# Performance work log

Measured on AMD Instinct MI355X. Metric: run time of the kernel, lower is better.

## Reference

```python
import jax, jax.numpy as jnp
import numpy as np

H = 1024
L = 2

def setup_inputs() -> dict:
    key = jax.random.key(0)
    k1, k2, k3, k4, k5 = jax.random.split(key, 5)
    B, S = 32, 2048
    scale = 1.0 / np.sqrt(H)
    return {
        "query": jax.random.normal(k1, (B, 1, H * L), dtype=jnp.float32),
        "keys": jax.random.normal(k2, (B, S, H), dtype=jnp.float32),
        "Wa_w": jax.random.normal(k3, (H * L, H), dtype=jnp.float32) * scale,
        "Wa_b": jnp.zeros((H,), dtype=jnp.float32),
        "Ua_w": jax.random.normal(k4, (H, H), dtype=jnp.float32) * scale,
        "Ua_b": jnp.zeros((H,), dtype=jnp.float32),
        "Va_w": jax.random.normal(k5, (H, 1), dtype=jnp.float32) * scale,
        "Va_b": jnp.zeros((1,), dtype=jnp.float32),
    }

def reference(query, keys, Wa_w, Wa_b, Ua_w, Ua_b, Va_w, Va_b):
    # query: [B,1,H*L], keys: [B,S,H]
    q = jnp.einsum('bqd,dh->bqh', query, Wa_w) + Wa_b   # [B,1,H]
    k = jnp.einsum('bsd,dh->bsh', keys, Ua_w) + Ua_b    # [B,S,H]
    e = jnp.tanh(q + k)                                  # [B,S,H]
    scores = jnp.einsum('bsh,ho->bso', e, Va_w) + Va_b   # [B,S,1]
    scores = scores[:, :, 0][:, None, :]                 # [B,1,S]
    weights = jax.nn.softmax(scores, axis=-1)            # [B,1,S]
    context = jnp.einsum('bqs,bsh->bqh', weights, keys)  # [B,1,H]
    return (context, weights)
```

## Files before the change

### kernel.cpp

```cpp
#include <hip/hip_runtime.h>
#include <hip/hip_bf16.h>


typedef __attribute__((ext_vector_type(8))) short short8;
typedef __attribute__((ext_vector_type(4))) float floatx4;

typedef const __attribute__((address_space(1))) unsigned int gu32;
typedef __attribute__((address_space(3))) unsigned int lu32;

__device__ __forceinline__ unsigned short f2bf(float f) {
    union { float f; unsigned int u; } c; c.f = f;
    unsigned int u = c.u + 0x7fffu + ((c.u >> 16) & 1u);
    return (unsigned short)(u >> 16);
}

__device__ __forceinline__ unsigned int f2bf2(float lo, float hi) {
#if __has_builtin(__builtin_amdgcn_cvt_pk_bf16_f32)
    auto r = __builtin_amdgcn_cvt_pk_bf16_f32(lo, hi);
    unsigned int u; __builtin_memcpy(&u, &r, 4);
    return u;
#else
    return (unsigned int)f2bf(lo) | ((unsigned int)f2bf(hi) << 16);
#endif
}

__device__ __forceinline__ void gld16(const unsigned short* g, unsigned short* l) {
    __builtin_amdgcn_global_load_lds(
        (gu32*)(uintptr_t)g,
        (lu32*)(unsigned int)(uintptr_t)l,
        16, 0, 0);
}

__global__ __launch_bounds__(256) void qproj_k(
    const float* __restrict__ query, const float* __restrict__ Wa,
    const float* __restrict__ Wab, const float* __restrict__ Uab,
    float* __restrict__ qws)
{
    __shared__ float qs[2048];
    __shared__ float red[16*64];
    const int tid = threadIdx.x;
    const int b = blockIdx.x, hc = blockIdx.y;
    #pragma unroll
    for (int i = 0; i < 8; i++) qs[tid + 256*i] = query[b*2048 + tid + 256*i];
    __syncthreads();
    const int hq = tid & 15;
    const int dg = tid >> 4;
    const float4* wp = reinterpret_cast<const float4*>(Wa + (size_t)(dg*128)*1024 + hc*64 + hq*4);
    const float* qp = qs + dg*128;
    float4 a0; a0.x = a0.y = a0.z = a0.w = 0.f;
    float4 a1; a1.x = a1.y = a1.z = a1.w = 0.f;
    #pragma unroll 4
    for (int d = 0; d < 128; d += 2) {
        float q0 = qp[d], q1 = qp[d+1];
        float4 w0 = wp[(size_t)d*256];
        float4 w1 = wp[(size_t)(d+1)*256];
        a0.x += q0*w0.x; a0.y += q0*w0.y; a0.z += q0*w0.z; a0.w += q0*w0.w;
        a1.x += q1*w1.x; a1.y += q1*w1.y; a1.z += q1*w1.z; a1.w += q1*w1.w;
    }
    a0.x += a1.x; a0.y += a1.y; a0.z += a1.z; a0.w += a1.w;
    *reinterpret_cast<float4*>(red + dg*64 + hq*4) = a0;
    __syncthreads();
    if (tid < 64) {
        float v = 0.f;
        #pragma unroll
        for (int g = 0; g < 16; g++) v += red[g*64 + tid];
        int hh = hc*64 + tid;
        qws[b*1024 + hh] = v + Wab[hh] + Uab[hh];
    }
}

__global__ __launch_bounds__(256) void uat_k(const float* __restrict__ Ua,
                                             unsigned short* __restrict__ uat)
{
    __shared__ unsigned short t[64][65];
    const int x = threadIdx.x & 63, yy = threadIdx.x >> 6;
    const int d0 = blockIdx.x*64, h0 = blockIdx.y*64;
    #pragma unroll
    for (int i = 0; i < 16; i++) {
        int y = yy*16 + i;
        t[y][x] = f2bf(Ua[(size_t)(d0+y)*1024 + h0 + x]);
    }
    __syncthreads();
    #pragma unroll
    for (int i = 0; i < 16; i++) {
        int y = yy*16 + i;
        uat[(size_t)(h0+y)*1024 + d0 + x] = t[x][y];
    }
}

__global__ __launch_bounds__(256) void kb16_k(const float* __restrict__ keys,
                                              unsigned short* __restrict__ kb)
{
    const size_t t = (size_t)blockIdx.x*256 + threadIdx.x;
    const size_t rg = t >> 5;
    const int g = (int)(t & 31);
    const int s = (int)(rg & 2047);
    const int p = (s >> 1) & 3;
    const float4* in4 = reinterpret_cast<const float4*>(keys + rg*1024 + g*32);
    uint4* out4 = reinterpret_cast<uint4*>(kb + rg*1024 + g*32);
    float4 v[8];
    #pragma unroll
    for (int q = 0; q < 8; q++) v[q] = in4[q];
    #pragma unroll
    for (int j = 0; j < 4; j++) {
        int jc = j ^ p;
        uint4 w;
        w.x = f2bf2(v[2*jc].x,   v[2*jc].y);
        w.y = f2bf2(v[2*jc].z,   v[2*jc].w);
        w.z = f2bf2(v[2*jc+1].x, v[2*jc+1].y);
        w.w = f2bf2(v[2*jc+1].z, v[2*jc+1].w);
        out4[j] = w;
    }
}

__global__ __launch_bounds__(256) void score_gemm_fast(
    const unsigned short* __restrict__ kb16,
    const unsigned short* __restrict__ uat,
    const float* __restrict__ qws,
    const float* __restrict__ Va,
    float* __restrict__ partial,
    int b0)
{
    __shared__ unsigned short aS[2][128*32];
    __shared__ unsigned short bS[2][128*32];
    const int tid = threadIdx.x;
    const int bz = blockIdx.z;
    const int b = b0 + bz;
    const int s0 = blockIdx.x * 128;
    const int h0 = blockIdx.y * 128;
    const int lane = tid & 63, wave = tid >> 6;
    const int quad = lane >> 4, l15 = lane & 15;
    const int wm = (wave & 1) * 64, wn = (wave >> 1) * 64;

    const int srow = lane >> 2;
    const int schunk = (lane & 3) ^ ((srow >> 1) & 3);
    const int c0 = wave*2, c1 = wave*2 + 1;
    const unsigned short* ubase = uat + (size_t)h0*1024;
    const size_t boff0 = (size_t)(c0*16 + srow)*1024 + schunk*8;
    const size_t boff1 = (size_t)(c1*16 + srow)*1024 + schunk*8;

    const unsigned short* kA = kb16 + (size_t)(bz*2048 + s0)*1024;
    const size_t aoff0 = (size_t)(tid >> 2)*1024 + (size_t)(tid & 3)*8;
    const size_t aoff1 = (size_t)(64 + (tid >> 2))*1024 + (size_t)(tid & 3)*8;

    floatx4 acc[4][4];
    #pragma unroll
    for (int i = 0; i < 4; i++)
        #pragma unroll
        for (int j = 0; j < 4; j++) acc[i][j] = (floatx4)0.0f;

    gld16(kA + aoff0,    aS[0] + wave*512);
    gld16(kA + aoff1,    aS[0] + 2048 + wave*512);
    gld16(ubase + boff0, bS[0] + c0*512);
    gld16(ubase + boff1, bS[0] + c1*512);
    __syncthreads();

    int cur = 0;
    for (int kt = 0; kt < 31; ++kt) {
        const int nxt = cur ^ 1;
        const int k1 = (kt + 1) << 5;

        gld16(kA + aoff0 + k1,    aS[nxt] + wave*512);
        gld16(kA + aoff1 + k1,    aS[nxt] + 2048 + wave*512);
        gld16(ubase + boff0 + k1, bS[nxt] + c0*512);
        gld16(ubase + boff1 + k1, bS[nxt] + c1*512);

        short8 af[4], bf8[4];
        #pragma unroll
        for (int i = 0; i < 4; i++) {
            int row = wm + 16*i + l15;
            af[i] = *reinterpret_cast<const short8*>(aS[cur] + row*32 + ((quad ^ ((row>>1)&3)) * 8));
        }
        #pragma unroll
        for (int j = 0; j < 4; j++) {
            int row = wn + 16*j + l15;
            bf8[j] = *reinterpret_cast<const short8*>(bS[cur] + row*32 + ((quad ^ ((row>>1)&3)) * 8));
        }
        #pragma unroll
        for (int i = 0; i < 4; i++)
            #pragma unroll
            for (int j = 0; j < 4; j++)
                acc[i][j] = __builtin_amdgcn_mfma_f32_16x16x32_bf16(af[i], bf8[j], acc[i][j], 0, 0, 0);

        __syncthreads();
        cur = nxt;
    }

    {
        short8 af[4], bf8[4];
        #pragma unroll
        for (int i = 0; i < 4; i++) {
            int row = wm + 16*i + l15;
            af[i] = *reinterpret_cast<const short8*>(aS[cur] + row*32 + ((quad ^ ((row>>1)&3)) * 8));
        }
        #pragma unroll
        for (int j = 0; j < 4; j++) {
            int row = wn + 16*j + l15;
            bf8[j] = *reinterpret_cast<const short8*>(bS[cur] + row*32 + ((quad ^ ((row>>1)&3)) * 8));
        }
        #pragma unroll
        for (int i = 0; i < 4; i++)
            #pragma unroll
            for (int j = 0; j < 4; j++)
                acc[i][j] = __builtin_amdgcn_mfma_f32_16x16x32_bf16(af[i], bf8[j], acc[i][j], 0, 0, 0);
    }

    float qv[4], vav[4];
    #pragma unroll
    for (int j = 0; j < 4; j++) {
        int n = h0 + wn + 16*j + l15;
        qv[j]  = qws[b*1024 + n];
        vav[j] = Va[n];
    }
    const int slot = blockIdx.y * 2 + (wave >> 1);
    #pragma unroll
    for (int i = 0; i < 4; i++) {
        #pragma unroll
        for (int r = 0; r < 4; r++) {
            float p = 0.f;
            #pragma unroll
            for (int j = 0; j < 4; j++) {
                float x = qv[j] + acc[i][j][r];
                float e = __expf(2.f * x);
                float t = 1.f - 2.f * __builtin_amdgcn_rcpf(e + 1.f);
                p += vav[j] * t;
            }
            #pragma unroll
            for (int off = 1; off < 16; off <<= 1) p += __shfl_xor(p, off, 64);
            if (l15 == 0) {
                int m = wm + 16*i + quad*4 + r;
                partial[((size_t)b*16 + slot)*2048 + s0 + m] = p;
            }
        }
    }
}

__global__ __launch_bounds__(256) void softmax_k(const float* __restrict__ partial,
                                                 float* __restrict__ out_w)
{
    const int tid = threadIdx.x;
    const int b = blockIdx.x;
    __shared__ float wred[4], wred2[4];
    float sc[8];
    float mx = -3.0e38f;
    #pragma unroll
    for (int i = 0; i < 8; i++) {
        int s = tid + 256*i;
        float v = 0.f;
        #pragma unroll
        for (int ht = 0; ht < 16; ht++) v += partial[((size_t)b*16 + ht)*2048 + s];
        sc[i] = v; mx = fmaxf(mx, v);
    }
    #pragma unroll
    for (int off = 32; off >= 1; off >>= 1) mx = fmaxf(mx, __shfl_xor(mx, off, 64));
    if ((tid & 63) == 0) wred[tid >> 6] = mx;
    __syncthreads();
    mx = fmaxf(fmaxf(wred[0], wred[1]), fmaxf(wred[2], wred[3]));
    float e[8]; float lsum = 0.f;
    #pragma unroll
    for (int i = 0; i < 8; i++) { e[i] = __expf(sc[i] - mx); lsum += e[i]; }
    #pragma unroll
    for (int off = 32; off >= 1; off >>= 1) lsum += __shfl_xor(lsum, off, 64);
    if ((tid & 63) == 0) wred2[tid >> 6] = lsum;
    __syncthreads();
    float inv = 1.0f / (wred2[0] + wred2[1] + wred2[2] + wred2[3]);
    #pragma unroll
    for (int i = 0; i < 8; i++) out_w[b*2048 + tid + 256*i] = e[i] * inv;
}

__global__ __launch_bounds__(256) void ctx_k(const float* __restrict__ keys,
                                             const float* __restrict__ w,
                                             float* __restrict__ ctxp, int sper)
{
    const int tid = threadIdx.x;
    const int b = blockIdx.x, sc = blockIdx.y;
    const float4* k4 = reinterpret_cast<const float4*>(keys) + (size_t)(b*2048 + sc*sper)*256;
    const float* wp = w + b*2048 + sc*sper;
    float4 a; a.x = a.y = a.z = a.w = 0.f;
    #pragma unroll 4
    for (int s = 0; s < sper; s++) {
        float wv = wp[s];
        float4 kv = k4[(size_t)s*256 + tid];
        a.x += wv*kv.x; a.y += wv*kv.y; a.z += wv*kv.z; a.w += wv*kv.w;
    }
    reinterpret_cast<float4*>(ctxp)[((size_t)b*gridDim.y + sc)*256 + tid] = a;
}

__global__ __launch_bounds__(256) void ctxsum_k(const float* __restrict__ ctxp,
                                                float* __restrict__ out, int nc)
{
    const int idx = blockIdx.x*256 + threadIdx.x;
    const int b = idx >> 10, h = idx & 1023;
    float v = 0.f;
    for (int s = 0; s < nc; s++) v += ctxp[((size_t)b*nc + s)*1024 + h];
    out[idx] = v;
}

extern "C" void kernel_launch(void* const* d_in, const int* in_sizes, int n_in,
                              void* d_out, int out_size, void* d_ws, size_t ws_size,
                              hipStream_t stream)
{
    const float* query = (const float*)d_in[0];
    const float* keys  = (const float*)d_in[1];
    const float* Wa_w  = (const float*)d_in[2];
    const float* Wa_b  = (const float*)d_in[3];
    const float* Ua_w  = (const float*)d_in[4];
    const float* Ua_b  = (const float*)d_in[5];
    const float* Va_w  = (const float*)d_in[6];

    char* ws = (char*)d_ws;
    float*          qws     = (float*)(ws);
    unsigned short* uat     = (unsigned short*)(ws + (131072));
    float*          partial = (float*)(ws + (131072 + 2097152));
    float*          ctxp    = (float*)(ws + (131072 + 2097152 + 4194304));
    const size_t BASE = 131072 + 2097152 + 4194304 + 2097152;
    unsigned short* kb16 = (unsigned short*)(ws + BASE);

    size_t avail = (ws_size > BASE) ? (ws_size - BASE) : 0;
    int nb = 32;
    while (nb > 1 && (size_t)nb * 2048 * 1024 * 2 > avail) nb >>= 1;

    float* out_ctx = (float*)d_out;
    float* out_w   = out_ctx + 32*1024;

    qproj_k<<<dim3(32, 16), 256, 0, stream>>>(query, Wa_w, Wa_b, Ua_b, qws);
    uat_k  <<<dim3(16, 16), 256, 0, stream>>>(Ua_w, uat);
    for (int b0 = 0; b0 < 32; b0 += nb) {
        kb16_k<<<dim3(nb*256), 256, 0, stream>>>(keys + (size_t)b0*2048*1024, kb16);
        score_gemm_fast<<<dim3(16, 8, nb), 256, 0, stream>>>(kb16, uat, qws, Va_w, partial, b0);
    }
    softmax_k<<<dim3(32),      256, 0, stream>>>(partial, out_w);
    ctx_k    <<<dim3(32, 16),  256, 0, stream>>>(keys, out_w, ctxp, 128);
    ctxsum_k <<<dim3(128),     256, 0, stream>>>(ctxp, out_ctx, 16);
}
```

Baseline: 725.5 us.

## Coalesce bf16 key conversion and accumulate scores with atomics instead of partials

The fp32-to-bf16 key conversion kernel now has each thread handle one float4 per iteration in a grid-stride style loop, with swizzled 8-byte stores, instead of one thread reading 32 contiguous floats. The aim is better coalescing of the large key stream. The score GEMM epilogue now atomically adds its per-row partial sums into a single zeroed score buffer rather than writing 16 partial slots. This removes the 16-way reduction reads in softmax, at the cost of atomic contention, an extra memset and non-deterministic summation order.

```diff
diff --git a/kernel.cpp b/kernel.cpp
--- a/kernel.cpp
+++ b/kernel.cpp
@@ -89,27 +89,28 @@
 }
 
 __global__ __launch_bounds__(256) void kb16_k(const float* __restrict__ keys,
-                                              unsigned short* __restrict__ kb)
-{
-    const size_t t = (size_t)blockIdx.x*256 + threadIdx.x;
-    const size_t rg = t >> 5;
-    const int g = (int)(t & 31);
-    const int s = (int)(rg & 2047);
-    const int p = (s >> 1) & 3;
-    const float4* in4 = reinterpret_cast<const float4*>(keys + rg*1024 + g*32);
-    uint4* out4 = reinterpret_cast<uint4*>(kb + rg*1024 + g*32);
-    float4 v[8];
-    #pragma unroll
-    for (int q = 0; q < 8; q++) v[q] = in4[q];
-    #pragma unroll
-    for (int j = 0; j < 4; j++) {
-        int jc = j ^ p;
-        uint4 w;
-        w.x = f2bf2(v[2*jc].x,   v[2*jc].y);
-        w.y = f2bf2(v[2*jc].z,   v[2*jc].w);
-        w.z = f2bf2(v[2*jc+1].x, v[2*jc+1].y);
-        w.w = f2bf2(v[2*jc+1].z, v[2*jc+1].w);
-        out4[j] = w;
+                                              unsigned short* __restrict__ kb,
+                                              unsigned int nf4)
+{
+    const unsigned int stride = gridDim.x * 256u;
+    unsigned int f = blockIdx.x * 256u + threadIdx.x;
+    #pragma unroll 4
+    for (int it = 0; it < 4; ++it, f += stride) {
+        if (f < nf4) {
+            unsigned int elem = f << 2;
+            unsigned int rg   = elem >> 10;
+            unsigned int rem  = elem & 1023u;
+            unsigned int g    = rem >> 5;
+            unsigned int c    = (rem >> 3) & 3u;
+            unsigned int half = (rem >> 2) & 1u;
+            unsigned int p    = ((rg & 2047u) >> 1) & 3u;
+            float4 v = reinterpret_cast<const float4*>(keys)[f];
+            uint2 w;
+            w.x = f2bf2(v.x, v.y);
+            w.y = f2bf2(v.z, v.w);
+            unsigned int dst = rg*1024u + g*32u + ((c ^ p) << 3) + (half << 2);
+            *reinterpret_cast<uint2*>(kb + dst) = w;
+        }
     }
 }
 
@@ -118,7 +119,7 @@
     const unsigned short* __restrict__ uat,
     const float* __restrict__ qws,
     const float* __restrict__ Va,
-    float* __restrict__ partial,
+    float* __restrict__ score,
     int b0)
 {
     __shared__ unsigned short aS[2][128*32];
@@ -212,7 +213,6 @@
         qv[j]  = qws[b*1024 + n];
         vav[j] = Va[n];
     }
-    const int slot = blockIdx.y * 2 + (wave >> 1);
     #pragma unroll
     for (int i = 0; i < 4; i++) {
         #pragma unroll
@@ -229,13 +229,13 @@
             for (int off = 1; off < 16; off <<= 1) p += __shfl_xor(p, off, 64);
             if (l15 == 0) {
                 int m = wm + 16*i + quad*4 + r;
-                partial[((size_t)b*16 + slot)*2048 + s0 + m] = p;
+                atomicAdd(score + (size_t)b*2048 + s0 + m, p);
             }
         }
     }
 }
 
-__global__ __launch_bounds__(256) void softmax_k(const float* __restrict__ partial,
+__global__ __launch_bounds__(256) void softmax_k(const float* __restrict__ score,
                                                  float* __restrict__ out_w)
 {
     const int tid = threadIdx.x;
@@ -245,11 +245,8 @@
     float mx = -3.0e38f;
     #pragma unroll
     for (int i = 0; i < 8; i++) {
-        int s = tid + 256*i;
-        float v = 0.f;
-        #pragma unroll
-        for (int ht = 0; ht < 16; ht++) v += partial[((size_t)b*16 + ht)*2048 + s];
-        sc[i] = v; mx = fmaxf(mx, v);
+        sc[i] = score[(size_t)b*2048 + tid + 256*i];
+        mx = fmaxf(mx, sc[i]);
     }
     #pragma unroll
     for (int off = 32; off >= 1; off >>= 1) mx = fmaxf(mx, __shfl_xor(mx, off, 64));
@@ -311,7 +308,7 @@
     char* ws = (char*)d_ws;
     float*          qws     = (float*)(ws);
     unsigned short* uat     = (unsigned short*)(ws + (131072));
-    float*          partial = (float*)(ws + (131072 + 2097152));
+    float*          score   = (float*)(ws + (131072 + 2097152));
     float*          ctxp    = (float*)(ws + (131072 + 2097152 + 4194304));
     const size_t BASE = 131072 + 2097152 + 4194304 + 2097152;
     unsigned short* kb16 = (unsigned short*)(ws + BASE);
@@ -323,13 +320,17 @@
     float* out_ctx = (float*)d_out;
     float* out_w   = out_ctx + 32*1024;
 
+    hipMemsetAsync(score, 0, 32*2048*sizeof(float), stream);
     qproj_k<<<dim3(32, 16), 256, 0, stream>>>(query, Wa_w, Wa_b, Ua_b, qws);
     uat_k  <<<dim3(16, 16), 256, 0, stream>>>(Ua_w, uat);
     for (int b0 = 0; b0 < 32; b0 += nb) {
-        kb16_k<<<dim3(nb*256), 256, 0, stream>>>(keys + (size_t)b0*2048*1024, kb16);
-        score_gemm_fast<<<dim3(16, 8, nb), 256, 0, stream>>>(kb16, uat, qws, Va_w, partial, b0);
-    }
-    softmax_k<<<dim3(32),      256, 0, stream>>>(partial, out_w);
+        unsigned int nf4 = (unsigned int)nb * 2048u * 256u;
+        unsigned int nthr = (nf4 + 3u) / 4u;
+        unsigned int nblk = (nthr + 255u) / 256u;
+        kb16_k<<<dim3(nblk), 256, 0, stream>>>(keys + (size_t)b0*2048*1024, kb16, nf4);
+        score_gemm_fast<<<dim3(16, 8, nb), 256, 0, stream>>>(kb16, uat, qws, Va_w, score, b0);
+    }
+    softmax_k<<<dim3(32),      256, 0, stream>>>(score, out_w);
     ctx_k    <<<dim3(32, 16),  256, 0, stream>>>(keys, out_w, ctxp, 128);
     ctxsum_k <<<dim3(128),     256, 0, stream>>>(ctxp, out_ctx, 16);
 }
```

Result: faster. 647.4 us (-10.8%).
